# Optimization experiments

Measured on AMD Instinct MI355X. Metric: run time of the kernel, lower is better.

Reference implementation:

```python
import jax, jax.numpy as jnp
import numpy as np

B, N, D = 8, 256, 128
EPS_AGG = 1e-6
LN_EPS = 1e-5


def setup_inputs() -> dict:
    key = jax.random.key(0)
    ks = jax.random.split(key, 12)
    s = lambda fan_in: 1.0 / np.sqrt(fan_in)
    inp = {
        "x": jax.random.normal(ks[0], (B, N, D), dtype=jnp.float32),
        "edge0": jax.random.normal(ks[1], (B, N, N, D), dtype=jnp.float32),
        "edge_mask": jax.random.randint(ks[2], (B, N, N), 0, 2, dtype=jnp.int32),
        # msg_mlp: Linear(3D->D), ReLU, Linear(D->D)
        "W1m": jax.random.uniform(ks[3], (3 * D, D), jnp.float32, -s(3 * D), s(3 * D)),
        "b1m": jax.random.uniform(ks[4], (D,), jnp.float32, -s(3 * D), s(3 * D)),
        "W2m": jax.random.uniform(ks[5], (D, D), jnp.float32, -s(D), s(D)),
        "b2m": jax.random.uniform(ks[6], (D,), jnp.float32, -s(D), s(D)),
        # upd_mlp: Linear(2D->D), ReLU, Linear(D->D)
        "W1u": jax.random.uniform(ks[7], (2 * D, D), jnp.float32, -s(2 * D), s(2 * D)),
        "b1u": jax.random.uniform(ks[8], (D,), jnp.float32, -s(2 * D), s(2 * D)),
        "W2u": jax.random.uniform(ks[9], (D, D), jnp.float32, -s(D), s(D)),
        "b2u": jax.random.uniform(ks[10], (D,), jnp.float32, -s(D), s(D)),
        # LayerNorm affine
        "gamma": jnp.ones((D,), jnp.float32),
        "beta": jnp.zeros((D,), jnp.float32),
    }
    return inp


def reference(x, edge0, edge_mask, W1m, b1m, W2m, b2m, W1u, b1u, W2u, b2u, gamma, beta):
    # All-pairs concat: [B, N_i, N_j, 3D]
    xi = jnp.broadcast_to(x[:, :, None, :], (B, N, N, D))
    xj = jnp.broadcast_to(x[:, None, :, :], (B, N, N, D))
    msg_in = jnp.concatenate([xi, xj, edge0], axis=-1)
    # 2-layer edge MLP
    h = jax.nn.relu(jnp.einsum("bijk,kd->bijd", msg_in, W1m) + b1m)
    msg = jnp.einsum("bijk,kd->bijd", h, W2m) + b2m
    # mask + mean-style aggregation over neighbors j
    m = edge_mask.astype(jnp.float32)
    agg = jnp.einsum("bijd,bij->bid", msg, m) / (m.sum(axis=2, keepdims=True) + EPS_AGG)
    # update MLP
    u_in = jnp.concatenate([x, agg], axis=-1)  # [B, N, 2D]
    hu = jax.nn.relu(u_in @ W1u + b1u)
    out = hu @ W2u + b2u
    # residual + LayerNorm
    y = x + out
    mu = y.mean(axis=-1, keepdims=True)
    var = y.var(axis=-1, keepdims=True)
    return (y - mu) * jax.lax.rsqrt(var + LN_EPS) * gamma + beta
```

## Files before the change

### kernel.cpp

```cpp
#include <hip/hip_runtime.h>
#include <hip/hip_bf16.h>

typedef float    f4    __attribute__((ext_vector_type(4)));
typedef short    s8v   __attribute__((ext_vector_type(8)));
typedef __bf16   bf8v  __attribute__((ext_vector_type(8)));
typedef unsigned int u32x4v __attribute__((ext_vector_type(4)));
typedef unsigned short u16;

typedef const __attribute__((address_space(1))) void GAS;
typedef __attribute__((address_space(3))) void LAS;

#define NB 8
#define NN 256
#define ND 128

static __device__ __forceinline__ u16 f2bf(float f) {
    union { float f; unsigned u; } v; v.f = f;
    unsigned r = v.u + 0x7FFF + ((v.u >> 16) & 1);
    return (u16)(r >> 16);
}

static __device__ __forceinline__ unsigned pack2bf(float a, float b) {
    unsigned ua = __builtin_bit_cast(unsigned, a) + 0x8000u;
    unsigned ub = __builtin_bit_cast(unsigned, b) + 0x8000u;
    return __builtin_amdgcn_perm(ub, ua, 0x07060302u);
}

__global__ __launch_bounds__(256) void prep_kernel(
    const float* __restrict__ x, const float* __restrict__ W1m,
    const float* __restrict__ b1m,
    float* __restrict__ P, float* __restrict__ Qt, u16* __restrict__ W1cp)
{
    if (blockIdx.x == 1024) {
        for (int idx = threadIdx.x; idx < 16384; idx += 256) {
            int e  = idx & 7;
            int ln = (idx >> 3) & 63;
            int nt = (idx >> 9) & 7;
            int kt = idx >> 12;
            int k  = kt * 32 + (ln >> 4) * 8 + e;
            int d  = nt * 16 + (ln & 15);
            W1cp[idx] = f2bf(W1m[(2 * ND + k) * ND + d]);
        }
        return;
    }
    __shared__ float xl[256];
    int t = threadIdx.x;
    int row0 = blockIdx.x * 2;
    xl[t] = x[row0 * ND + t];
    __syncthreads();
    int r = t >> 7;
    int d = t & 127;
    int row = row0 + r;
    float sp = b1m[d], sq = 0.f;
    const float* xr = &xl[r * ND];
    #pragma unroll 8
    for (int k = 0; k < ND; ++k) {
        float xv = xr[k];
        sp += xv * W1m[k * ND + d];
        sq += xv * W1m[(ND + k) * ND + d];
    }
    P[row * ND + d] = sp;
    Qt[((size_t)((row >> 8) * ND + d)) * NN + (row & 255)] = sq;
}

__global__ __launch_bounds__(256, 4) void fused_kernel(
    const float* __restrict__ x, const float* __restrict__ edge0,
    const int* __restrict__ mask,
    const float* __restrict__ W2m, const float* __restrict__ b2m,
    const float* __restrict__ W1u, const float* __restrict__ b1u,
    const float* __restrict__ W2u, const float* __restrict__ b2u,
    const float* __restrict__ gamma, const float* __restrict__ beta,
    const float* __restrict__ P, const float* __restrict__ Qt,
    const u16* __restrict__ W1cp,
    float* __restrict__ out)
{
    __shared__ float ebuf[2][32 * 128];
    __shared__ float ml[NN];
    __shared__ float aggH[ND];
    __shared__ float xrow[ND];
    __shared__ float am[ND];
    __shared__ float hu[ND];
    __shared__ float yl[ND];
    __shared__ float redc[4], redA[4], redB[4];

    const int bid  = blockIdx.x;
    const int b    = bid >> 8;
    const int tid  = threadIdx.x;
    const int wave = tid >> 6;
    const int lane = tid & 63;
    const int l15  = lane & 15;
    const int lg   = lane >> 4;

    const char* e0c = (const char*)(edge0 + (size_t)bid * (NN * ND));

    float mval = (float)mask[bid * NN + tid];
    ml[tid] = mval;
    if (tid < ND) xrow[tid] = x[bid * ND + tid];

    s8v bfr[4][2];
    #pragma unroll
    for (int kt = 0; kt < 4; ++kt)
        #pragma unroll
        for (int n = 0; n < 2; ++n)
            bfr[kt][n] = *reinterpret_cast<const s8v*>(
                &W1cp[(((kt * 8) + (wave * 2 + n)) * 64 + lane) * 8]);

    const int col0 = wave * 32 + l15;
    const float pv0 = P[bid * ND + col0];
    const float pv1 = P[bid * ND + col0 + 16];
    const float* qt0 = Qt + (size_t)(b * ND + col0) * NN;
    const float* qt1 = qt0 + (size_t)16 * NN;

    auto STAGE = [&](int cc, int bb) {
        const char* cb = e0c + (size_t)cc * 16384;
        #pragma unroll
        for (int u = 0; u < 4; ++u) {
            int row  = wave * 8 + u * 2 + (lane >> 5);
            int colb = (lane & 31) * 16;
            const char* g = cb + row * 512 + (colb ^ ((row & 7) << 4));
            __builtin_amdgcn_global_load_lds(
                (GAS*)g, (LAS*)&ebuf[bb][(wave * 4 + u) * 256], 16, 0, 0);
        }
    };

    float agg0 = 0.f, agg1 = 0.f;
    f4 q0r[2][2], q1r[2][2];

    #pragma unroll
    for (int m = 0; m < 2; ++m) {
        int j0 = m * 16 + lg * 4;
        q0r[0][m] = *reinterpret_cast<const f4*>(qt0 + j0);
        q1r[0][m] = *reinterpret_cast<const f4*>(qt1 + j0);
    }
    __builtin_amdgcn_sched_barrier(0);
    STAGE(0, 0);
    __builtin_amdgcn_sched_barrier(0);

    #pragma unroll
    for (int c = 0; c < 8; ++c) {
        const int pb = c & 1, nb = pb ^ 1;
        if (c < 7) {
            #pragma unroll
            for (int m = 0; m < 2; ++m) {
                int j0 = (c + 1) * 32 + m * 16 + lg * 4;
                q0r[nb][m] = *reinterpret_cast<const f4*>(qt0 + j0);
                q1r[nb][m] = *reinterpret_cast<const f4*>(qt1 + j0);
            }
            __builtin_amdgcn_sched_barrier(0);
            STAGE(c + 1, nb);
            __builtin_amdgcn_sched_barrier(0);
            asm volatile("s_waitcnt vmcnt(8) lgkmcnt(0)" ::: "memory");
        } else {
            asm volatile("s_waitcnt vmcnt(0) lgkmcnt(0)" ::: "memory");
        }
        __builtin_amdgcn_s_barrier();
        __builtin_amdgcn_sched_barrier(0);

        const char* bufc = (const char*)&ebuf[pb][0];
        #pragma unroll
        for (int m = 0; m < 2; ++m) {
            f4 acc0 = {0.f, 0.f, 0.f, 0.f};
            f4 acc1 = {0.f, 0.f, 0.f, 0.f};
            int row = m * 16 + l15;
            int rb  = row * 512;
            int swz = (row & 7) << 4;
            #pragma unroll
            for (int kt = 0; kt < 4; ++kt) {
                int cbyte = kt * 128 + lg * 32;
                f4 a0 = *reinterpret_cast<const f4*>(bufc + rb + ((cbyte)      ^ swz));
                f4 a1 = *reinterpret_cast<const f4*>(bufc + rb + ((cbyte + 16) ^ swz));
                u32x4v aw;
                aw[0] = pack2bf(a0[0], a0[1]);
                aw[1] = pack2bf(a0[2], a0[3]);
                aw[2] = pack2bf(a1[0], a1[1]);
                aw[3] = pack2bf(a1[2], a1[3]);
                bf8v av = __builtin_bit_cast(bf8v, aw);
                acc0 = __builtin_amdgcn_mfma_f32_16x16x32_bf16(
                    av, __builtin_bit_cast(bf8v, bfr[kt][0]), acc0, 0, 0, 0);
                acc1 = __builtin_amdgcn_mfma_f32_16x16x32_bf16(
                    av, __builtin_bit_cast(bf8v, bfr[kt][1]), acc1, 0, 0, 0);
            }
            int j0 = c * 32 + m * 16 + lg * 4;
            f4 q0 = q0r[pb][m];
            f4 q1 = q1r[pb][m];
            #pragma unroll
            for (int r = 0; r < 4; ++r) {
                float mm = ml[j0 + r];
                float h0 = fmaxf(acc0[r] + pv0 + q0[r], 0.f);
                float h1 = fmaxf(acc1[r] + pv1 + q1[r], 0.f);
                agg0 += mm * h0;
                agg1 += mm * h1;
            }
        }
        __builtin_amdgcn_sched_barrier(0);
        __builtin_amdgcn_s_barrier();
    }

    agg0 += __shfl_xor(agg0, 16); agg0 += __shfl_xor(agg0, 32);
    agg1 += __shfl_xor(agg1, 16); agg1 += __shfl_xor(agg1, 32);
    if (lg == 0) {
        aggH[wave * 32 + l15]      = agg0;
        aggH[wave * 32 + 16 + l15] = agg1;
    }
    float cv = mval;
    #pragma unroll
    for (int o = 32; o > 0; o >>= 1) cv += __shfl_xor(cv, o);
    if (lane == 0) redc[wave] = cv;
    __syncthreads();

    const float cnt = redc[0] + redc[1] + redc[2] + redc[3];
    const float inv = 1.f / (cnt + 1e-6f);
    const int d  = tid & 127;
    const int hf = tid >> 7;

    {
        float s = 0.f;
        #pragma unroll 8
        for (int k = hf * 64; k < hf * 64 + 64; ++k) s += aggH[k] * W2m[k * ND + d];
        ml[tid] = s;
    }
    __syncthreads();
    if (tid < ND) am[d] = (ml[d] + ml[d + ND] + cnt * b2m[d]) * inv;
    __syncthreads();
    {
        float s = 0.f;
        const float* W = W1u + (size_t)hf * ND * ND;
        const float* v = hf ? am : xrow;
        #pragma unroll 8
        for (int k = 0; k < ND; ++k) s += v[k] * W[k * ND + d];
        ml[tid] = s;
    }
    __syncthreads();
    if (tid < ND) hu[d] = fmaxf(ml[d] + ml[d + ND] + b1u[d], 0.f);
    __syncthreads();
    {
        float s = 0.f;
        #pragma unroll 8
        for (int k = hf * 64; k < hf * 64 + 64; ++k) s += hu[k] * W2u[k * ND + d];
        ml[tid] = s;
    }
    __syncthreads();
    if (tid < ND) yl[d] = xrow[d] + ml[d] + ml[d + ND] + b2u[d];
    __syncthreads();
    float yv = (tid < ND) ? yl[tid] : 0.f;
    float s1 = yv, s2 = yv * yv;
    #pragma unroll
    for (int o = 32; o > 0; o >>= 1) { s1 += __shfl_xor(s1, o); s2 += __shfl_xor(s2, o); }
    if (lane == 0) { redA[wave] = s1; redB[wave] = s2; }
    __syncthreads();
    if (tid < ND) {
        float mu  = (redA[0] + redA[1] + redA[2] + redA[3]) * (1.f / 128.f);
        float ex2 = (redB[0] + redB[1] + redB[2] + redB[3]) * (1.f / 128.f);
        float var = ex2 - mu * mu;
        float rs  = rsqrtf(var + 1e-5f);
        out[bid * ND + d] = (yl[d] - mu) * rs * gamma[d] + beta[d];
    }
}

extern "C" void kernel_launch(void* const* d_in, const int* in_sizes, int n_in,
                              void* d_out, int out_size, void* d_ws, size_t ws_size,
                              hipStream_t stream) {
    (void)in_sizes; (void)n_in; (void)out_size; (void)ws_size;
    const float* x     = (const float*)d_in[0];
    const float* edge0 = (const float*)d_in[1];
    const int*   mask  = (const int*)d_in[2];
    const float* W1m   = (const float*)d_in[3];
    const float* b1m   = (const float*)d_in[4];
    const float* W2m   = (const float*)d_in[5];
    const float* b2m   = (const float*)d_in[6];
    const float* W1u   = (const float*)d_in[7];
    const float* b1u   = (const float*)d_in[8];
    const float* W2u   = (const float*)d_in[9];
    const float* b2u   = (const float*)d_in[10];
    const float* gamma = (const float*)d_in[11];
    const float* beta  = (const float*)d_in[12];

    float* P    = (float*)d_ws;
    float* Qt   = P + 2048 * 128;
    u16*   W1cp = (u16*)(Qt + 8 * 128 * 256);

    float* o = (float*)d_out;

    prep_kernel<<<dim3(1025), dim3(256), 0, stream>>>(x, W1m, b1m, P, Qt, W1cp);
    fused_kernel<<<dim3(2048), dim3(256), 0, stream>>>(
        x, edge0, mask, W2m, b2m, W1u, b1u, W2u, b2u, gamma, beta,
        P, Qt, W1cp, o);
}
```

Measured before the change: 101.0 us.

## Load edge tiles directly into registers, dropping LDS staging and block barriers

Replaces the LDS double-buffered staging of edge0 tiles (global_load_lds plus s_barrier) with per-wave direct global-to-register loads, double-buffered in VGPRs over 16 steps of 16 rows. Each wave now loads the full 16x128 tile it needs itself, so all four waves redundantly fetch the same edge rows. This removes LDS traffic and the block-wide barriers. It also remaps block IDs so consecutive blocks come from different batches, and lowers launch bounds occupancy to 2 to allow more registers. The cost is 4x redundant global/L2 reads of edge0 per block and lower occupancy.

```diff
diff --git a/kernel.cpp b/kernel.cpp
--- a/kernel.cpp
+++ b/kernel.cpp
@@ -6,9 +6,6 @@
 typedef __bf16   bf8v  __attribute__((ext_vector_type(8)));
 typedef unsigned int u32x4v __attribute__((ext_vector_type(4)));
 typedef unsigned short u16;
-
-typedef const __attribute__((address_space(1))) void GAS;
-typedef __attribute__((address_space(3))) void LAS;
 
 #define NB 8
 #define NN 256
@@ -63,7 +60,7 @@
     Qt[((size_t)((row >> 8) * ND + d)) * NN + (row & 255)] = sq;
 }
 
-__global__ __launch_bounds__(256, 4) void fused_kernel(
+__global__ __launch_bounds__(256, 2) void fused_kernel(
     const float* __restrict__ x, const float* __restrict__ edge0,
     const int* __restrict__ mask,
     const float* __restrict__ W2m, const float* __restrict__ b2m,
@@ -74,16 +71,12 @@
     const u16* __restrict__ W1cp,
     float* __restrict__ out)
 {
-    __shared__ float ebuf[2][32 * 128];
     __shared__ float ml[NN];
-    __shared__ float aggH[ND];
     __shared__ float xrow[ND];
-    __shared__ float am[ND];
-    __shared__ float hu[ND];
-    __shared__ float yl[ND];
+    __shared__ float aggH[ND], am[ND], hu[ND], yl[ND];
     __shared__ float redc[4], redA[4], redB[4];
 
-    const int bid  = blockIdx.x;
+    const int bid  = (blockIdx.x & 7) * 256 + (blockIdx.x >> 3);
     const int b    = bid >> 8;
     const int tid  = threadIdx.x;
     const int wave = tid >> 6;
@@ -92,6 +85,7 @@
     const int lg   = lane >> 4;
 
     const char* e0c = (const char*)(edge0 + (size_t)bid * (NN * ND));
+    const char* erow = e0c + l15 * 512 + lg * 32;
 
     float mval = (float)mask[bid * NN + tid];
     ml[tid] = mval;
@@ -108,92 +102,78 @@
     const int col0 = wave * 32 + l15;
     const float pv0 = P[bid * ND + col0];
     const float pv1 = P[bid * ND + col0 + 16];
-    const float* qt0 = Qt + (size_t)(b * ND + col0) * NN;
+    const float* qt0 = Qt + (size_t)(b * ND + col0) * NN + lg * 4;
     const float* qt1 = qt0 + (size_t)16 * NN;
 
-    auto STAGE = [&](int cc, int bb) {
-        const char* cb = e0c + (size_t)cc * 16384;
-        #pragma unroll
-        for (int u = 0; u < 4; ++u) {
-            int row  = wave * 8 + u * 2 + (lane >> 5);
-            int colb = (lane & 31) * 16;
-            const char* g = cb + row * 512 + (colb ^ ((row & 7) << 4));
-            __builtin_amdgcn_global_load_lds(
-                (GAS*)g, (LAS*)&ebuf[bb][(wave * 4 + u) * 256], 16, 0, 0);
-        }
-    };
-
     float agg0 = 0.f, agg1 = 0.f;
-    f4 q0r[2][2], q1r[2][2];
-
-    #pragma unroll
-    for (int m = 0; m < 2; ++m) {
-        int j0 = m * 16 + lg * 4;
-        q0r[0][m] = *reinterpret_cast<const f4*>(qt0 + j0);
-        q1r[0][m] = *reinterpret_cast<const f4*>(qt1 + j0);
+
+    __syncthreads();
+
+    f4 eA[2][8];
+    f4 qA[2][2];
+
+    {
+        qA[0][0] = *reinterpret_cast<const f4*>(qt0);
+        qA[0][1] = *reinterpret_cast<const f4*>(qt1);
+        #pragma unroll
+        for (int kt = 0; kt < 4; ++kt) {
+            eA[0][2 * kt]     = *reinterpret_cast<const f4*>(erow + kt * 128);
+            eA[0][2 * kt + 1] = *reinterpret_cast<const f4*>(erow + kt * 128 + 16);
+        }
     }
     __builtin_amdgcn_sched_barrier(0);
-    STAGE(0, 0);
-    __builtin_amdgcn_sched_barrier(0);
-
-    #pragma unroll
-    for (int c = 0; c < 8; ++c) {
-        const int pb = c & 1, nb = pb ^ 1;
-        if (c < 7) {
+
+    #pragma unroll
+    for (int t = 0; t < 16; ++t) {
+        const int cur = t & 1, nxt = cur ^ 1;
+        if (t < 15) {
+            const char* er = erow + (size_t)(t + 1) * 8192;
+            qA[nxt][0] = *reinterpret_cast<const f4*>(qt0 + (t + 1) * 16);
+            qA[nxt][1] = *reinterpret_cast<const f4*>(qt1 + (t + 1) * 16);
             #pragma unroll
-            for (int m = 0; m < 2; ++m) {
-                int j0 = (c + 1) * 32 + m * 16 + lg * 4;
-                q0r[nb][m] = *reinterpret_cast<const f4*>(qt0 + j0);
-                q1r[nb][m] = *reinterpret_cast<const f4*>(qt1 + j0);
+            for (int kt = 0; kt < 4; ++kt) {
+                eA[nxt][2 * kt]     = *reinterpret_cast<const f4*>(er + kt * 128);
+                eA[nxt][2 * kt + 1] = *reinterpret_cast<const f4*>(er + kt * 128 + 16);
             }
             __builtin_amdgcn_sched_barrier(0);
-            STAGE(c + 1, nb);
+            asm volatile("s_waitcnt vmcnt(10)" ::: "memory");
+        } else {
             __builtin_amdgcn_sched_barrier(0);
-            asm volatile("s_waitcnt vmcnt(8) lgkmcnt(0)" ::: "memory");
-        } else {
-            asm volatile("s_waitcnt vmcnt(0) lgkmcnt(0)" ::: "memory");
-        }
-        __builtin_amdgcn_s_barrier();
+            asm volatile("s_waitcnt vmcnt(0)" ::: "memory");
+        }
         __builtin_amdgcn_sched_barrier(0);
 
-        const char* bufc = (const char*)&ebuf[pb][0];
-        #pragma unroll
-        for (int m = 0; m < 2; ++m) {
-            f4 acc0 = {0.f, 0.f, 0.f, 0.f};
-            f4 acc1 = {0.f, 0.f, 0.f, 0.f};
-            int row = m * 16 + l15;
-            int rb  = row * 512;
-            int swz = (row & 7) << 4;
-            #pragma unroll
-            for (int kt = 0; kt < 4; ++kt) {
-                int cbyte = kt * 128 + lg * 32;
-                f4 a0 = *reinterpret_cast<const f4*>(bufc + rb + ((cbyte)      ^ swz));
-                f4 a1 = *reinterpret_cast<const f4*>(bufc + rb + ((cbyte + 16) ^ swz));
-                u32x4v aw;
-                aw[0] = pack2bf(a0[0], a0[1]);
-                aw[1] = pack2bf(a0[2], a0[3]);
-                aw[2] = pack2bf(a1[0], a1[1]);
-                aw[3] = pack2bf(a1[2], a1[3]);
-                bf8v av = __builtin_bit_cast(bf8v, aw);
-                acc0 = __builtin_amdgcn_mfma_f32_16x16x32_bf16(
-                    av, __builtin_bit_cast(bf8v, bfr[kt][0]), acc0, 0, 0, 0);
-                acc1 = __builtin_amdgcn_mfma_f32_16x16x32_bf16(
-                    av, __builtin_bit_cast(bf8v, bfr[kt][1]), acc1, 0, 0, 0);
-            }
-            int j0 = c * 32 + m * 16 + lg * 4;
-            f4 q0 = q0r[pb][m];
-            f4 q1 = q1r[pb][m];
-            #pragma unroll
-            for (int r = 0; r < 4; ++r) {
-                float mm = ml[j0 + r];
-                float h0 = fmaxf(acc0[r] + pv0 + q0[r], 0.f);
-                float h1 = fmaxf(acc1[r] + pv1 + q1[r], 0.f);
-                agg0 += mm * h0;
-                agg1 += mm * h1;
-            }
-        }
-        __builtin_amdgcn_sched_barrier(0);
-        __builtin_amdgcn_s_barrier();
+        s8v apk[4];
+        #pragma unroll
+        for (int kt = 0; kt < 4; ++kt) {
+            f4 a0 = eA[cur][2 * kt];
+            f4 a1 = eA[cur][2 * kt + 1];
+            u32x4v aw;
+            aw[0] = pack2bf(a0[0], a0[1]);
+            aw[1] = pack2bf(a0[2], a0[3]);
+            aw[2] = pack2bf(a1[0], a1[1]);
+            aw[3] = pack2bf(a1[2], a1[3]);
+            apk[kt] = __builtin_bit_cast(s8v, aw);
+        }
+        f4 acc0 = {0.f, 0.f, 0.f, 0.f};
+        f4 acc1 = {0.f, 0.f, 0.f, 0.f};
+        #pragma unroll
+        for (int kt = 0; kt < 4; ++kt) {
+            acc0 = __builtin_amdgcn_mfma_f32_16x16x32_bf16(
+                __builtin_bit_cast(bf8v, apk[kt]), __builtin_bit_cast(bf8v, bfr[kt][0]), acc0, 0, 0, 0);
+            acc1 = __builtin_amdgcn_mfma_f32_16x16x32_bf16(
+                __builtin_bit_cast(bf8v, apk[kt]), __builtin_bit_cast(bf8v, bfr[kt][1]), acc1, 0, 0, 0);
+        }
+        f4 mk = *reinterpret_cast<const f4*>(&ml[t * 16 + lg * 4]);
+        f4 q0 = qA[cur][0];
+        f4 q1 = qA[cur][1];
+        #pragma unroll
+        for (int r = 0; r < 4; ++r) {
+            float h0 = fmaxf(acc0[r] + pv0 + q0[r], 0.f);
+            float h1 = fmaxf(acc1[r] + pv1 + q1[r], 0.f);
+            agg0 += mk[r] * h0;
+            agg1 += mk[r] * h1;
+        }
     }
 
     agg0 += __shfl_xor(agg0, 16); agg0 += __shfl_xor(agg0, 32);
```

Measured after the change: 193.4 us. 91.5% more time.
